# Optimization experiments

Hardware: AMD Instinct MI355X
Metric: run time of the kernel (lower is better)

The kernel has to match this reference:

```python
import jax, jax.numpy as jnp
import numpy as np

IN_FEATURES = 4096
OUT_FEATURES = 4096
GROUPS = 1
QB = 2 ** (8 - 1) - 1  # 127, int8 absmax quant


def setup_inputs() -> dict:
    key = jax.random.key(0)
    k_x, k_w = jax.random.split(key)
    x = jax.random.normal(k_x, (8192, IN_FEATURES), dtype=jnp.float32)
    # kaiming_uniform_(a=sqrt(5)) -> uniform(-1/sqrt(in), 1/sqrt(in))
    bound = 1.0 / np.sqrt(IN_FEATURES)
    weight = jax.random.uniform(
        k_w, (OUT_FEATURES, IN_FEATURES), dtype=jnp.float32,
        minval=-bound, maxval=bound)
    return {"input": x, "weight": weight}


def reference(input, weight):
    # --- ternarize weight per group ---
    w = weight.reshape(GROUPS, -1)                       # [G, out*in/G]
    w = w - jnp.mean(w, axis=1, keepdims=True)
    w = jnp.sign(w)
    # beta: per-group scale (note denominator uses full element count, as in source)
    beta = jnp.sum(jnp.abs(w), axis=1, keepdims=True) / (w.shape[0] * w.shape[1])
    w = (w * beta).reshape(OUT_FEATURES, IN_FEATURES)    # [out, in]

    # --- absmax int8 quantize activations (quantized values used, not dequant) ---
    scale = QB / jnp.max(jnp.abs(input))
    quant = jnp.round(scale * input)                     # [tokens, in]

    # --- linear + rescale ---
    out = quant @ w.T                                    # [tokens, out]
    out = out / beta.reshape(-1, 1)                      # groups=1: scalar divide
    return out
```

## Files before the change

kernel.cpp:

```cpp
#include <hip/hip_runtime.h>
#include <hip/hip_bf16.h>

typedef __attribute__((ext_vector_type(4))) int int4v;

#define TOKENS 8192
#define IN_F   4096
#define OUT_F  4096


__global__ __launch_bounds__(256) void k_pre(const float4* __restrict__ w,
                                             const float4* __restrict__ x,
                                             double* __restrict__ partials,
                                             float* __restrict__ xpart) {
  if (blockIdx.x < 1024) {
    __shared__ double sm[256];
    double s = 0.0;
    const float4* p = w + (size_t)blockIdx.x * 4096;
    for (int i = threadIdx.x; i < 4096; i += 256) {
      float4 v = p[i];
      s += (double)v.x + (double)v.y + (double)v.z + (double)v.w;
    }
    sm[threadIdx.x] = s;
    __syncthreads();
    for (int off = 128; off > 0; off >>= 1) {
      if (threadIdx.x < off) sm[threadIdx.x] += sm[threadIdx.x + off];
      __syncthreads();
    }
    if (threadIdx.x == 0) partials[blockIdx.x] = sm[0];
  } else {
    const int b = blockIdx.x - 1024;
    float m = 0.f;
    const size_t n = (size_t)TOKENS * IN_F / 4;
    for (size_t i = (size_t)b * 256 + threadIdx.x; i < n; i += (size_t)1024 * 256) {
      float4 v = x[i];
      m = fmaxf(m, fmaxf(fmaxf(fabsf(v.x), fabsf(v.y)),
                         fmaxf(fabsf(v.z), fabsf(v.w))));
    }
    __shared__ float smf[256];
    smf[threadIdx.x] = m;
    __syncthreads();
    for (int off = 128; off > 0; off >>= 1) {
      if (threadIdx.x < off) smf[threadIdx.x] = fmaxf(smf[threadIdx.x], smf[threadIdx.x + off]);
      __syncthreads();
    }
    if (threadIdx.x == 0) xpart[b] = smf[0];
  }
}

__global__ __launch_bounds__(256) void k_finalize(double* __restrict__ hdr,
                                                  const double* __restrict__ partials,
                                                  const float* __restrict__ xpart) {
  __shared__ double sm[256];
  __shared__ float smf[256];
  double s = partials[threadIdx.x] + partials[threadIdx.x + 256] +
             partials[threadIdx.x + 512] + partials[threadIdx.x + 768];
  float m = fmaxf(fmaxf(xpart[threadIdx.x], xpart[threadIdx.x + 256]),
                  fmaxf(xpart[threadIdx.x + 512], xpart[threadIdx.x + 768]));
  sm[threadIdx.x] = s;
  smf[threadIdx.x] = m;
  __syncthreads();
  for (int off = 128; off > 0; off >>= 1) {
    if (threadIdx.x < off) {
      sm[threadIdx.x] += sm[threadIdx.x + off];
      smf[threadIdx.x] = fmaxf(smf[threadIdx.x], smf[threadIdx.x + off]);
    }
    __syncthreads();
  }
  if (threadIdx.x == 0) {
    hdr[0] = sm[0] / (double)((size_t)OUT_F * IN_F);
    hdr[1] = 127.0 / (double)smf[0];
  }
}

#define QB_BLK ((TOKENS * IN_F / 4) / 256)
#define TB_BLK ((OUT_F * IN_F / 4) / 256)
__global__ __launch_bounds__(256) void k_quant_tern(const float4* __restrict__ x,
                                                    const float4* __restrict__ w,
                                                    int* __restrict__ q,
                                                    int* __restrict__ sgn,
                                                    const double* __restrict__ hdr) {
  if (blockIdx.x < QB_BLK) {
    const double s = hdr[1];
    size_t i = (size_t)blockIdx.x * 256 + threadIdx.x;
    float4 v = x[i];
    int a = (int)rint(s * (double)v.x);
    int b = (int)rint(s * (double)v.y);
    int c = (int)rint(s * (double)v.z);
    int d = (int)rint(s * (double)v.w);
    q[i] = (a & 255) | ((b & 255) << 8) | ((c & 255) << 16) | ((d & 255) << 24);
  } else {
    const double m = hdr[0];
    size_t i = (size_t)(blockIdx.x - QB_BLK) * 256 + threadIdx.x;
    float4 v = w[i];
    int a = ((double)v.x > m) - ((double)v.x < m);
    int b = ((double)v.y > m) - ((double)v.y < m);
    int c = ((double)v.z > m) - ((double)v.z < m);
    int d = ((double)v.w > m) - ((double)v.w < m);
    sgn[i] = (a & 255) | ((b & 255) << 8) | ((c & 255) << 16) | ((d & 255) << 24);
  }
}

__device__ __forceinline__ void stageA(const signed char* __restrict__ gsrc,
                                       size_t grow0, int ktile,
                                       signed char* ldsbase, int tid, int wid) {
#pragma unroll
  for (int i = 0; i < 2; ++i) {
    const int slot = i * 512 + tid;
    const int r = slot >> 2;
    const int sir = slot & 3;
    const signed char* g = gsrc + (grow0 + (size_t)r) * IN_F +
                           (size_t)ktile * 64 + ((sir ^ ((r >> 1) & 3)) << 4);
    __builtin_amdgcn_global_load_lds(
        (const __attribute__((address_space(1))) void*)g,
        (__attribute__((address_space(3))) void*)(ldsbase + (i * 512 + wid * 64) * 16),
        16, 0, 0);
  }
}

__device__ __forceinline__ void stageB(const signed char* __restrict__ gsrc,
                                       size_t grow0, int ktile,
                                       signed char* ldsbase, int tid, int wid) {
  const int r = tid >> 2;
  const int sir = tid & 3;
  const signed char* g = gsrc + (grow0 + (size_t)r) * IN_F +
                         (size_t)ktile * 64 + ((sir ^ ((r >> 1) & 3)) << 4);
  __builtin_amdgcn_global_load_lds(
      (const __attribute__((address_space(1))) void*)g,
      (__attribute__((address_space(3))) void*)(ldsbase + (wid * 64) * 16),
      16, 0, 0);
}

__global__ __launch_bounds__(512, 4) void k_gemm(const signed char* __restrict__ q,
                                                 const signed char* __restrict__ s,
                                                 float* __restrict__ out) {
  __shared__ signed char sA[2][256 * 64];
  __shared__ signed char sB[2][128 * 64];
  const int tid  = threadIdx.x;
  const int lane = tid & 63;
  const int wid  = tid >> 6;
  const int wm   = wid >> 1;
  const int wn   = wid & 1;
  const int l15  = lane & 15, l4 = lane >> 4;

  const int swz = (blockIdx.x & 7) * 128 + (blockIdx.x >> 3);
  const int bm = swz >> 5;
  const int bn = swz & 31;
  const size_t row0 = (size_t)bm * 256;
  const size_t col0 = (size_t)bn * 128;

  const int lane_off = l15 * 64 + ((l4 ^ ((l15 >> 1) & 3)) << 4);

  int4v acc[4][4];
#pragma unroll
  for (int i = 0; i < 4; ++i)
#pragma unroll
    for (int j = 0; j < 4; ++j) acc[i][j] = int4v{0, 0, 0, 0};

  stageA(q, row0, 0, sA[0], tid, wid);
  stageB(s, col0, 0, sB[0], tid, wid);
  asm volatile("s_waitcnt vmcnt(0)" ::: "memory");
  __builtin_amdgcn_sched_barrier(0);
  __builtin_amdgcn_s_barrier();
  __builtin_amdgcn_sched_barrier(0);

  for (int kt = 0; kt < 64; ++kt) {
    const int c = kt & 1;
    const signed char* bufA = sA[c];
    const signed char* bufB = sB[c];

    if (kt != 63) {
      stageA(q, row0, kt + 1, sA[c ^ 1], tid, wid);
      stageB(s, col0, kt + 1, sB[c ^ 1], tid, wid);
    }
    __builtin_amdgcn_sched_barrier(0);

    int4v a[4], b[4];
#pragma unroll
    for (int f = 0; f < 4; ++f)
      a[f] = *(const int4v*)(bufA + (wm * 64 + f * 16) * 64 + lane_off);
#pragma unroll
    for (int f = 0; f < 4; ++f)
      b[f] = *(const int4v*)(bufB + (wn * 64 + f * 16) * 64 + lane_off);
    asm volatile("s_waitcnt lgkmcnt(0)" ::: "memory");
    __builtin_amdgcn_sched_barrier(0);
    __builtin_amdgcn_s_setprio(1);
#pragma unroll
    for (int fm = 0; fm < 4; ++fm)
#pragma unroll
      for (int fn = 0; fn < 4; ++fn)
        acc[fm][fn] = __builtin_amdgcn_mfma_i32_16x16x64_i8(a[fm], b[fn], acc[fm][fn], 0, 0, 0);
    __builtin_amdgcn_s_setprio(0);
    __builtin_amdgcn_sched_barrier(0);
    asm volatile("s_waitcnt vmcnt(0)" ::: "memory");
    __builtin_amdgcn_sched_barrier(0);
    __builtin_amdgcn_s_barrier();
    __builtin_amdgcn_sched_barrier(0);
  }

#pragma unroll
  for (int fm = 0; fm < 4; ++fm)
#pragma unroll
    for (int fn = 0; fn < 4; ++fn)
#pragma unroll
      for (int r = 0; r < 4; ++r) {
        const size_t rg = row0 + wm * 64 + fm * 16 + l4 * 4 + r;
        const size_t cg = col0 + wn * 64 + fn * 16 + l15;
        out[rg * OUT_F + cg] = (float)acc[fm][fn][r];
      }
}

extern "C" void kernel_launch(void* const* d_in, const int* in_sizes, int n_in,
                              void* d_out, int out_size, void* d_ws, size_t ws_size,
                              hipStream_t stream) {
  const float* x = (const float*)d_in[0];
  const float* w = (const float*)d_in[1];
  float* out = (float*)d_out;

  char* ws = (char*)d_ws;
  double*   hdr      = (double*)ws;
  double*   partials = (double*)(ws + 1024);
  float*    xpart    = (float*)(ws + 9216);
  signed char* qbuf  = (signed char*)(ws + 16384);
  signed char* sbuf  = (signed char*)(ws + 16384 + (size_t)TOKENS * IN_F);

  k_pre<<<2048, 256, 0, stream>>>((const float4*)w, (const float4*)x, partials, xpart);
  k_finalize<<<1, 256, 0, stream>>>(hdr, partials, xpart);
  k_quant_tern<<<QB_BLK + TB_BLK, 256, 0, stream>>>((const float4*)x, (const float4*)w,
                                                    (int*)qbuf, (int*)sbuf, hdr);
  k_gemm<<<(TOKENS / 256) * (OUT_F / 128), 512, 0, stream>>>(qbuf, sbuf, out);
}
```

Measured before the change: 231.1 us.

## Enlarge GEMM tile to 256x256, load B directly to registers, triple-buffer A

The int8 GEMM block tile grows from 256x128 to 256x256, and each of the 8 waves now computes a 128x64 sub-tile with 8x4 accumulators. The B operand no longer goes through LDS: each wave loads its B fragments straight from global memory into registers, one k-tile ahead. A is staged into LDS with three buffers, so loads run two k-tiles ahead. The aim is to cut global and LDS traffic per MFMA and overlap loads with compute better, at the cost of more registers, lower occupancy (launch bounds 2), and fewer blocks (512).

```diff
diff --git a/kernel.cpp b/kernel.cpp
--- a/kernel.cpp
+++ b/kernel.cpp
@@ -117,95 +117,96 @@
   }
 }
 
-__device__ __forceinline__ void stageB(const signed char* __restrict__ gsrc,
-                                       size_t grow0, int ktile,
-                                       signed char* ldsbase, int tid, int wid) {
-  const int r = tid >> 2;
-  const int sir = tid & 3;
-  const signed char* g = gsrc + (grow0 + (size_t)r) * IN_F +
-                         (size_t)ktile * 64 + ((sir ^ ((r >> 1) & 3)) << 4);
-  __builtin_amdgcn_global_load_lds(
-      (const __attribute__((address_space(1))) void*)g,
-      (__attribute__((address_space(3))) void*)(ldsbase + (wid * 64) * 16),
-      16, 0, 0);
-}
-
-__global__ __launch_bounds__(512, 4) void k_gemm(const signed char* __restrict__ q,
+__global__ __launch_bounds__(512, 2) void k_gemm(const signed char* __restrict__ q,
                                                  const signed char* __restrict__ s,
                                                  float* __restrict__ out) {
-  __shared__ signed char sA[2][256 * 64];
-  __shared__ signed char sB[2][128 * 64];
+  __shared__ signed char sA[3][256 * 64];
   const int tid  = threadIdx.x;
   const int lane = tid & 63;
   const int wid  = tid >> 6;
-  const int wm   = wid >> 1;
-  const int wn   = wid & 1;
+  const int wm   = wid >> 2;
+  const int wn   = wid & 3;
   const int l15  = lane & 15, l4 = lane >> 4;
 
-  const int swz = (blockIdx.x & 7) * 128 + (blockIdx.x >> 3);
-  const int bm = swz >> 5;
-  const int bn = swz & 31;
+  const int swz = (blockIdx.x & 7) * 64 + (blockIdx.x >> 3);
+  const int bm = swz >> 4;
+  const int bn = swz & 15;
   const size_t row0 = (size_t)bm * 256;
-  const size_t col0 = (size_t)bn * 128;
+  const size_t col0 = (size_t)bn * 256;
 
   const int lane_off = l15 * 64 + ((l4 ^ ((l15 >> 1) & 3)) << 4);
 
-  int4v acc[4][4];
-#pragma unroll
-  for (int i = 0; i < 4; ++i)
+  const signed char* bptr = s + (col0 + (size_t)(wn * 64 + l15)) * IN_F + l4 * 16;
+
+  int4v acc[8][4];
+#pragma unroll
+  for (int i = 0; i < 8; ++i)
 #pragma unroll
     for (int j = 0; j < 4; ++j) acc[i][j] = int4v{0, 0, 0, 0};
 
+  int4v bc[4], bnx[4];
+
   stageA(q, row0, 0, sA[0], tid, wid);
-  stageB(s, col0, 0, sB[0], tid, wid);
-  asm volatile("s_waitcnt vmcnt(0)" ::: "memory");
+  __builtin_amdgcn_sched_barrier(0);
+#pragma unroll
+  for (int f = 0; f < 4; ++f)
+    bnx[f] = *(const int4v*)(bptr + (size_t)f * 16 * IN_F);
+  __builtin_amdgcn_sched_barrier(0);
+  stageA(q, row0, 1, sA[1], tid, wid);
+  __builtin_amdgcn_sched_barrier(0);
+  asm volatile("s_waitcnt vmcnt(2)" ::: "memory");
   __builtin_amdgcn_sched_barrier(0);
   __builtin_amdgcn_s_barrier();
   __builtin_amdgcn_sched_barrier(0);
-
+#pragma unroll
+  for (int f = 0; f < 4; ++f) bc[f] = bnx[f];
+
+  int cur = 0, stg = 2;
   for (int kt = 0; kt < 64; ++kt) {
-    const int c = kt & 1;
-    const signed char* bufA = sA[c];
-    const signed char* bufB = sB[c];
-
-    if (kt != 63) {
-      stageA(q, row0, kt + 1, sA[c ^ 1], tid, wid);
-      stageB(s, col0, kt + 1, sB[c ^ 1], tid, wid);
-    }
-    __builtin_amdgcn_sched_barrier(0);
-
-    int4v a[4], b[4];
+    const signed char* bufA = sA[cur];
+
+    const int bt = (kt + 1) & 63;
 #pragma unroll
     for (int f = 0; f < 4; ++f)
-      a[f] = *(const int4v*)(bufA + (wm * 64 + f * 16) * 64 + lane_off);
-#pragma unroll
-    for (int f = 0; f < 4; ++f)
-      b[f] = *(const int4v*)(bufB + (wn * 64 + f * 16) * 64 + lane_off);
+      bnx[f] = *(const int4v*)(bptr + (size_t)f * 16 * IN_F + bt * 64);
+    __builtin_amdgcn_sched_barrier(0);
+    stageA(q, row0, (kt + 2) & 63, sA[stg], tid, wid);
+    __builtin_amdgcn_sched_barrier(0);
+
+    int4v a[8];
+#pragma unroll
+    for (int m = 0; m < 8; ++m)
+      a[m] = *(const int4v*)(bufA + (wm * 128 + m * 16) * 64 + lane_off);
     asm volatile("s_waitcnt lgkmcnt(0)" ::: "memory");
     __builtin_amdgcn_sched_barrier(0);
     __builtin_amdgcn_s_setprio(1);
 #pragma unroll
-    for (int fm = 0; fm < 4; ++fm)
-#pragma unroll
-      for (int fn = 0; fn < 4; ++fn)
-        acc[fm][fn] = __builtin_amdgcn_mfma_i32_16x16x64_i8(a[fm], b[fn], acc[fm][fn], 0, 0, 0);
+    for (int m = 0; m < 8; ++m)
+#pragma unroll
+      for (int n = 0; n < 4; ++n)
+        acc[m][n] = __builtin_amdgcn_mfma_i32_16x16x64_i8(a[m], bc[n], acc[m][n], 0, 0, 0);
     __builtin_amdgcn_s_setprio(0);
     __builtin_amdgcn_sched_barrier(0);
-    asm volatile("s_waitcnt vmcnt(0)" ::: "memory");
+    asm volatile("s_waitcnt vmcnt(2)" ::: "memory");
     __builtin_amdgcn_sched_barrier(0);
     __builtin_amdgcn_s_barrier();
     __builtin_amdgcn_sched_barrier(0);
-  }
-
-#pragma unroll
-  for (int fm = 0; fm < 4; ++fm)
-#pragma unroll
-    for (int fn = 0; fn < 4; ++fn)
+#pragma unroll
+    for (int f = 0; f < 4; ++f) bc[f] = bnx[f];
+
+    cur = (cur == 2) ? 0 : cur + 1;
+    stg = (stg == 2) ? 0 : stg + 1;
+  }
+
+#pragma unroll
+  for (int m = 0; m < 8; ++m)
+#pragma unroll
+    for (int n = 0; n < 4; ++n)
 #pragma unroll
       for (int r = 0; r < 4; ++r) {
-        const size_t rg = row0 + wm * 64 + fm * 16 + l4 * 4 + r;
-        const size_t cg = col0 + wn * 64 + fn * 16 + l15;
-        out[rg * OUT_F + cg] = (float)acc[fm][fn][r];
+        const size_t rg = row0 + wm * 128 + m * 16 + l4 * 4 + r;
+        const size_t cg = col0 + wn * 64 + n * 16 + l15;
+        out[rg * OUT_F + cg] = (float)acc[m][n][r];
       }
 }
 
@@ -227,5 +228,5 @@
   k_finalize<<<1, 256, 0, stream>>>(hdr, partials, xpart);
   k_quant_tern<<<QB_BLK + TB_BLK, 256, 0, stream>>>((const float4*)x, (const float4*)w,
                                                     (int*)qbuf, (int*)sbuf, hdr);
-  k_gemm<<<(TOKENS / 256) * (OUT_F / 128), 512, 0, stream>>>(qbuf, sbuf, out);
-}
+  k_gemm<<<(TOKENS / 256) * (OUT_F / 256), 512, 0, stream>>>(qbuf, sbuf, out);
+}
```

Result: slower. 312.4 us (+35.2%).
